# Kernel tuning notes

Hardware: AMD Instinct MI355X
Metric: run time of the kernel (lower is better)

## Reference

```python
import jax, jax.numpy as jnp
import numpy as np

N = 100000   # nodes
E = 1600000  # edges (avg degree 16)
F_IN, H, C = 128, 64, 40


def setup_inputs() -> dict:
    key = jax.random.key(0)
    ks = jax.random.split(key, 10)
    s = 0.05
    return {
        "x": jax.random.normal(ks[0], (N, F_IN), jnp.float32),
        "edge_index": jax.random.randint(ks[1], (2, E), 0, N, dtype=jnp.int32),
        "W0": jax.random.normal(ks[2], (F_IN, H), jnp.float32) * s,
        "b0": jnp.zeros((H,), jnp.float32),
        "W1": jax.random.normal(ks[3], (H, H), jnp.float32) * s,
        "b1": jnp.zeros((H,), jnp.float32),
        "W2": jax.random.normal(ks[4], (H, H), jnp.float32) * s,
        "b2": jnp.zeros((H,), jnp.float32),
        "W3": jax.random.normal(ks[5], (H, C), jnp.float32) * s,
        "b3": jnp.zeros((C,), jnp.float32),
    }


def reference(x, edge_index, W0, b0, W1, b1, W2, b2, W3, b3):
    # PyG GCNConv: add self-loops, symmetric normalization deg^-1/2 A deg^-1/2.
    loops = jnp.arange(N, dtype=edge_index.dtype)
    src = jnp.concatenate([edge_index[0], loops])  # message sources (x_j)
    dst = jnp.concatenate([edge_index[1], loops])  # aggregation targets
    deg = jax.ops.segment_sum(jnp.ones_like(dst, dtype=x.dtype), dst, num_segments=N)
    dinv = jnp.where(deg > 0, jax.lax.rsqrt(deg), 0.0)
    norm = dinv[src] * dinv[dst]  # [E+N]

    def conv(h, W, b):
        h = h @ W                                   # transform first (fewer bytes moved)
        msg = h[src] * norm[:, None]                # gather + scale
        return jax.ops.segment_sum(msg, dst, num_segments=N) + b

    h = jax.nn.leaky_relu(conv(x, W0, b0))
    h = jax.nn.leaky_relu(conv(h, W1, b1))
    h = jax.nn.leaky_relu(conv(h, W2, b2))
    h = conv(h, W3, b3)
    return jax.nn.softmax(h, axis=1)
```

## Files before the change

kernel.cpp:

```cpp
#include <hip/hip_runtime.h>
#include <hip/hip_fp16.h>
#include <math.h>


#define BBITS 9
#define BSIZE 512
#define BCAP 10240
#define CHUNK 2048
#define STAGE_CAP 12288

typedef __attribute__((ext_vector_type(8))) _Float16 half8;
typedef __attribute__((ext_vector_type(4))) float f32x4;

__global__ __launch_bounds__(256) void passA_kernel(const int* __restrict__ src, const int* __restrict__ dst,
                                                    int* gCursor, unsigned* __restrict__ pairbuf,
                                                    int nE, int nPassA,
                                                    const float* __restrict__ W0, const float* __restrict__ W1,
                                                    const float* __restrict__ W2, const float* __restrict__ W3,
                                                    __half* __restrict__ Wt0, __half* __restrict__ Wt1,
                                                    __half* __restrict__ Wt2, __half* __restrict__ Wt3) {
    const int t = threadIdx.x;
    if (blockIdx.x >= nPassA) {
        const int b = blockIdx.x - nPassA;
        if (b < 3) {
            const float* W = (b == 0) ? W0 : (b == 1) ? W1 : W2;
            __half* Wt = (b == 0) ? Wt0 : (b == 1) ? Wt1 : Wt2;
            const int K = (b == 0) ? 128 : 64;
            const int tot = 64 * K;
            for (int i = t; i < tot; i += 256) {
                int nn = i / K, k = i - nn * K;
                Wt[i] = (__half)W[k * 64 + nn];
            }
        } else {
            for (int i = t; i < 48 * 64; i += 256) {
                int c = i >> 6, k = i & 63;
                Wt3[i] = (c < 40) ? (__half)W3[k * 40 + c] : (__half)0.f;
            }
        }
        return;
    }
    __shared__ int hist[256], base[256], offs[256];
    hist[t] = 0; offs[t] = 0;
    __syncthreads();
    const int e0 = blockIdx.x * CHUNK;
    #pragma unroll
    for (int i = 0; i < CHUNK / 256; ++i) {
        int e = e0 + i * 256 + t;
        if (e < nE) atomicAdd(&hist[dst[e] >> BBITS], 1);
    }
    __syncthreads();
    if (hist[t]) base[t] = atomicAdd(&gCursor[t], hist[t]);
    __syncthreads();
    #pragma unroll
    for (int i = 0; i < CHUNK / 256; ++i) {
        int e = e0 + i * 256 + t;
        if (e < nE) {
            int d = dst[e];
            int b = d >> BBITS;
            int pos = b * BCAP + base[b] + atomicAdd(&offs[b], 1);
            pairbuf[pos] = (unsigned)src[e] | ((unsigned)(d & (BSIZE - 1)) << 17);
        }
    }
}

__global__ __launch_bounds__(256) void passB_kernel(const unsigned* __restrict__ pairbuf, const int* __restrict__ gCursor,
                                                    int* __restrict__ rowbeg, int* __restrict__ rowend,
                                                    float* __restrict__ dinv, int* __restrict__ adj, int n) {
    __shared__ unsigned stage[STAGE_CAP];
    __shared__ int cnt[BSIZE], rb[BSIZE], cur[BSIZE];
    __shared__ int sb[256];
    const int t = threadIdx.x;
    const int b = blockIdx.x;
    const int pBeg = b * BCAP;
    const int m = gCursor[b];
    cnt[t] = 0; cnt[t + 256] = 0; cur[t] = 0; cur[t + 256] = 0;
    __syncthreads();
    const bool useStage = (m <= STAGE_CAP);
    for (int i = t; i < m; i += 256) {
        unsigned p = pairbuf[pBeg + i];
        if (useStage) stage[i] = p;
        atomicAdd(&cnt[p >> 17], 1);
    }
    __syncthreads();
    const int c0 = cnt[2 * t], c1 = cnt[2 * t + 1];
    const int pairSum = c0 + c1;
    sb[t] = pairSum;
    __syncthreads();
    for (int off = 1; off < 256; off <<= 1) {
        int u = (t >= off) ? sb[t - off] : 0;
        __syncthreads();
        sb[t] += u;
        __syncthreads();
    }
    const int excl = sb[t] - pairSum;
    rb[2 * t] = excl;
    rb[2 * t + 1] = excl + c0;
    __syncthreads();
    const int nodeBase = b << BBITS;
    for (int local = t; local < BSIZE; local += 256) {
        int node = nodeBase + local;
        if (node < n) {
            int beg = pBeg + rb[local];
            rowbeg[node] = beg;
            rowend[node] = beg + cnt[local];
            dinv[node] = rsqrtf((float)(cnt[local] + 1));
        }
    }
    for (int i = t; i < m; i += 256) {
        unsigned p = useStage ? stage[i] : pairbuf[pBeg + i];
        int local = (int)(p >> 17);
        int s = (int)(p & 0x1FFFF);
        int pos = pBeg + rb[local] + atomicAdd(&cur[local], 1);
        adj[pos] = s;
    }
}

template<int K, bool AF32>
__global__ __launch_bounds__(256) void gemm_mfma_kernel(const void* __restrict__ Xv, const __half* __restrict__ Wt,
                                                        const float* __restrict__ dinv, __half* __restrict__ T, int n) {
    __shared__ __half sOut[4][16][72];
    const int tid = threadIdx.x;
    const int w = tid >> 6;
    const int l = tid & 63;
    const int l15 = l & 15;
    const int kg = l >> 4;
    const int rowBase = blockIdx.x * 64 + w * 16;

    f32x4 acc0 = {0.f, 0.f, 0.f, 0.f};
    f32x4 acc1 = acc0, acc2 = acc0, acc3 = acc0;

    const int m = rowBase + l15;
    const int mc = (m < n) ? m : (n - 1);

    for (int kc = 0; kc < K / 32; ++kc) {
        const int kb = kc * 32 + kg * 8;
        half8 a;
        if constexpr (AF32) {
            const float* Xp = (const float*)Xv + (long)mc * K + kb;
            const float4 f0 = *reinterpret_cast<const float4*>(Xp);
            const float4 f1 = *reinterpret_cast<const float4*>(Xp + 4);
            a[0] = (_Float16)f0.x; a[1] = (_Float16)f0.y; a[2] = (_Float16)f0.z; a[3] = (_Float16)f0.w;
            a[4] = (_Float16)f1.x; a[5] = (_Float16)f1.y; a[6] = (_Float16)f1.z; a[7] = (_Float16)f1.w;
        } else {
            a = *reinterpret_cast<const half8*>((const __half*)Xv + (long)mc * K + kb);
        }
        const half8 b0 = *reinterpret_cast<const half8*>(Wt + (long)(0 * 16 + l15) * K + kb);
        const half8 b1 = *reinterpret_cast<const half8*>(Wt + (long)(1 * 16 + l15) * K + kb);
        const half8 b2 = *reinterpret_cast<const half8*>(Wt + (long)(2 * 16 + l15) * K + kb);
        const half8 b3 = *reinterpret_cast<const half8*>(Wt + (long)(3 * 16 + l15) * K + kb);
        acc0 = __builtin_amdgcn_mfma_f32_16x16x32_f16(a, b0, acc0, 0, 0, 0);
        acc1 = __builtin_amdgcn_mfma_f32_16x16x32_f16(a, b1, acc1, 0, 0, 0);
        acc2 = __builtin_amdgcn_mfma_f32_16x16x32_f16(a, b2, acc2, 0, 0, 0);
        acc3 = __builtin_amdgcn_mfma_f32_16x16x32_f16(a, b3, acc3, 0, 0, 0);
    }

    float di[4];
    #pragma unroll
    for (int r = 0; r < 4; ++r) {
        const int mr = rowBase + kg * 4 + r;
        di[r] = dinv[(mr < n) ? mr : (n - 1)];
    }
    #pragma unroll
    for (int r = 0; r < 4; ++r) {
        sOut[w][kg * 4 + r][0 * 16 + l15] = (__half)(acc0[r] * di[r]);
        sOut[w][kg * 4 + r][1 * 16 + l15] = (__half)(acc1[r] * di[r]);
        sOut[w][kg * 4 + r][2 * 16 + l15] = (__half)(acc2[r] * di[r]);
        sOut[w][kg * 4 + r][3 * 16 + l15] = (__half)(acc3[r] * di[r]);
    }
    __syncthreads();
    const int srow = l >> 2;
    const int scol = (l & 3) * 16;
    const int gm = rowBase + srow;
    if (gm < n) {
        const uint4 q0 = *reinterpret_cast<const uint4*>(&sOut[w][srow][scol]);
        const uint4 q1 = *reinterpret_cast<const uint4*>(&sOut[w][srow][scol + 8]);
        *reinterpret_cast<uint4*>(&T[(long)gm * 64 + scol]) = q0;
        *reinterpret_cast<uint4*>(&T[(long)gm * 64 + scol + 8]) = q1;
    }
}

__global__ __launch_bounds__(256) void gemm3_mfma_kernel(const __half* __restrict__ X, const __half* __restrict__ Wt3,
                                                         const float* __restrict__ dinv, __half* __restrict__ T3, int n) {
    __shared__ __half sOut[4][16][72];
    const int tid = threadIdx.x;
    const int w = tid >> 6;
    const int l = tid & 63;
    const int l15 = l & 15;
    const int kg = l >> 4;
    const int rowBase = blockIdx.x * 64 + w * 16;

    f32x4 acc0 = {0.f, 0.f, 0.f, 0.f};
    f32x4 acc1 = acc0, acc2 = acc0;
    const int m = rowBase + l15;
    const int mc = (m < n) ? m : (n - 1);

    #pragma unroll
    for (int kc = 0; kc < 2; ++kc) {
        const int kb = kc * 32 + kg * 8;
        const half8 a = *reinterpret_cast<const half8*>(X + (long)mc * 64 + kb);
        const half8 b0 = *reinterpret_cast<const half8*>(Wt3 + (long)(0 * 16 + l15) * 64 + kb);
        const half8 b1 = *reinterpret_cast<const half8*>(Wt3 + (long)(1 * 16 + l15) * 64 + kb);
        const half8 b2 = *reinterpret_cast<const half8*>(Wt3 + (long)(2 * 16 + l15) * 64 + kb);
        acc0 = __builtin_amdgcn_mfma_f32_16x16x32_f16(a, b0, acc0, 0, 0, 0);
        acc1 = __builtin_amdgcn_mfma_f32_16x16x32_f16(a, b1, acc1, 0, 0, 0);
        acc2 = __builtin_amdgcn_mfma_f32_16x16x32_f16(a, b2, acc2, 0, 0, 0);
    }

    float di[4];
    #pragma unroll
    for (int r = 0; r < 4; ++r) {
        const int mr = rowBase + kg * 4 + r;
        di[r] = dinv[(mr < n) ? mr : (n - 1)];
    }
    #pragma unroll
    for (int r = 0; r < 4; ++r) {
        sOut[w][kg * 4 + r][0 * 16 + l15] = (__half)(acc0[r] * di[r]);
        sOut[w][kg * 4 + r][1 * 16 + l15] = (__half)(acc1[r] * di[r]);
        sOut[w][kg * 4 + r][2 * 16 + l15] = (__half)(acc2[r] * di[r]);
    }
    __syncthreads();
    const int srow = l >> 2;
    const int p = l & 3;
    const int gm = rowBase + srow;
    if (gm < n) {
        const uint4 q = *reinterpret_cast<const uint4*>(&sOut[w][srow][p * 8]);
        *reinterpret_cast<uint4*>(&T3[(long)gm * 40 + p * 8]) = q;
        if (p == 0) {
            const uint4 q2 = *reinterpret_cast<const uint4*>(&sOut[w][srow][32]);
            *reinterpret_cast<uint4*>(&T3[(long)gm * 40 + 32]) = q2;
        }
    }
}

__device__ __forceinline__ void accum_row(const uint4& r, __half2& x0, __half2& x1, __half2& x2, __half2& x3) {
    const __half2* v = reinterpret_cast<const __half2*>(&r);
    x0 = __hadd2(x0, v[0]); x1 = __hadd2(x1, v[1]);
    x2 = __hadd2(x2, v[2]); x3 = __hadd2(x3, v[3]);
}

template<int CHS, bool SOFTMAX>
__global__ __launch_bounds__(256) void agg_kernel(const __half* __restrict__ Tp, const float* __restrict__ dinv,
                                                  const int* __restrict__ rowbeg, const int* __restrict__ rowend,
                                                  const int* __restrict__ adj,
                                                  const float* __restrict__ bias, void* __restrict__ outp, int n) {
    const int tid = threadIdx.x;
    const int c = tid & 7;
    const int d = (int)((blockIdx.x * 256 + tid) >> 3);
    if (d >= n) return;
    const bool act = (CHS == 8) || (c < CHS);
    const int cc = act ? c : (CHS - 1);
    const uint4* Tp4 = reinterpret_cast<const uint4*>(Tp);

    __half2 a0 = __float2half2_rn(0.f), a1 = a0, a2 = a0, a3 = a0;
    __half2 c0 = a0, c1 = a0, c2 = a0, c3 = a0;
    const int beg = rowbeg[d], end = rowend[d];

    int e0 = beg;
    for (; e0 + 8 <= end; e0 += 8) {
        const int myadj = adj[e0 + c];
        uint4 r[8];
        #pragma unroll
        for (int j = 0; j < 8; ++j) {
            const int s = __shfl(myadj, j, 8);
            r[j] = Tp4[(long)s * CHS + cc];
        }
        accum_row(r[0], a0, a1, a2, a3);
        accum_row(r[1], c0, c1, c2, c3);
        accum_row(r[2], a0, a1, a2, a3);
        accum_row(r[3], c0, c1, c2, c3);
        accum_row(r[4], a0, a1, a2, a3);
        accum_row(r[5], c0, c1, c2, c3);
        accum_row(r[6], a0, a1, a2, a3);
        accum_row(r[7], c0, c1, c2, c3);
    }
    if (e0 < end) {
        const int last = end - 1;
        const int idx = e0 + c;
        const int myadj = adj[idx <= last ? idx : last];
        uint4 r[8];
        #pragma unroll
        for (int j = 0; j < 8; ++j) {
            const int s = __shfl(myadj, j, 8);
            r[j] = Tp4[(long)s * CHS + cc];
        }
        #pragma unroll
        for (int j = 0; j < 8; ++j) {
            if (e0 + j <= last) {
                if (j & 1) accum_row(r[j], c0, c1, c2, c3);
                else       accum_row(r[j], a0, a1, a2, a3);
            }
        }
    }

    float vals[8];
    if (act) {
        const uint4 sraw = Tp4[(long)d * CHS + c];
        const __half2* sh = reinterpret_cast<const __half2*>(&sraw);
        a0 = __hadd2(__hadd2(a0, c0), sh[0]);
        a1 = __hadd2(__hadd2(a1, c1), sh[1]);
        a2 = __hadd2(__hadd2(a2, c2), sh[2]);
        a3 = __hadd2(__hadd2(a3, c3), sh[3]);
        const float di = dinv[d];
        const float4 b0 = *reinterpret_cast<const float4*>(&bias[c * 8]);
        const float4 b1 = *reinterpret_cast<const float4*>(&bias[c * 8 + 4]);
        const float2 f0 = __half22float2(a0), f1 = __half22float2(a1);
        const float2 f2 = __half22float2(a2), f3 = __half22float2(a3);
        vals[0] = f0.x * di + b0.x; vals[1] = f0.y * di + b0.y;
        vals[2] = f1.x * di + b0.z; vals[3] = f1.y * di + b0.w;
        vals[4] = f2.x * di + b1.x; vals[5] = f2.y * di + b1.y;
        vals[6] = f3.x * di + b1.z; vals[7] = f3.y * di + b1.w;
    }

    if constexpr (!SOFTMAX) {
        if (act) {
            union { __half h[8]; uint4 u; } p;
            #pragma unroll
            for (int j = 0; j < 8; ++j) {
                const float v = vals[j];
                p.h[j] = (__half)(v > 0.f ? v : 0.01f * v);
            }
            *reinterpret_cast<uint4*>(&((__half*)outp)[(long)d * 64 + c * 8]) = p.u;
        }
    } else {
        float mx = -1e30f;
        if (act) {
            #pragma unroll
            for (int j = 0; j < 8; ++j) mx = fmaxf(mx, vals[j]);
        }
        #pragma unroll
        for (int off = 1; off <= 4; off <<= 1) mx = fmaxf(mx, __shfl_xor(mx, off, 8));
        float e8[8];
        float sum = 0.f;
        if (act) {
            #pragma unroll
            for (int j = 0; j < 8; ++j) { e8[j] = expf(vals[j] - mx); sum += e8[j]; }
        }
        #pragma unroll
        for (int off = 1; off <= 4; off <<= 1) sum += __shfl_xor(sum, off, 8);
        if (act) {
            const float inv = 1.0f / sum;
            float* out = (float*)outp;
            const float4 o0 = make_float4(e8[0] * inv, e8[1] * inv, e8[2] * inv, e8[3] * inv);
            const float4 o1 = make_float4(e8[4] * inv, e8[5] * inv, e8[6] * inv, e8[7] * inv);
            *reinterpret_cast<float4*>(&out[(long)d * 40 + c * 8]) = o0;
            *reinterpret_cast<float4*>(&out[(long)d * 40 + c * 8 + 4]) = o1;
        }
    }
}

extern "C" void kernel_launch(void* const* d_in, const int* in_sizes, int n_in,
                              void* d_out, int out_size, void* d_ws, size_t ws_size,
                              hipStream_t stream) {
    const float* x  = (const float*)d_in[0];
    const int*   ei = (const int*)d_in[1];
    const float* W0 = (const float*)d_in[2];
    const float* b0 = (const float*)d_in[3];
    const float* W1 = (const float*)d_in[4];
    const float* b1 = (const float*)d_in[5];
    const float* W2 = (const float*)d_in[6];
    const float* b2 = (const float*)d_in[7];
    const float* W3 = (const float*)d_in[8];
    const float* b3 = (const float*)d_in[9];

    const int N = in_sizes[0] / 128;
    const int E = in_sizes[1] / 2;
    const int* src = ei;
    const int* dst = ei + E;

    const int nBuck = (N + BSIZE - 1) >> BBITS;

    char* ws = (char*)d_ws;
    auto align256 = [](size_t v) { return (v + 255) & ~(size_t)255; };
    size_t o = 0;
    int*    gCursor    = (int*)(ws + o);    o += align256(256 * 4);
    int*    rowbeg     = (int*)(ws + o);    o += align256((size_t)N * 4);
    int*    rowend     = (int*)(ws + o);    o += align256((size_t)N * 4);
    float*  dinv       = (float*)(ws + o);  o += align256((size_t)N * 4);
    int*    adj        = (int*)(ws + o);    o += align256((size_t)nBuck * BCAP * 4);
    __half* Wt0        = (__half*)(ws + o); o += align256(64 * 128 * 2);
    __half* Wt1        = (__half*)(ws + o); o += align256(64 * 64 * 2);
    __half* Wt2        = (__half*)(ws + o); o += align256(64 * 64 * 2);
    __half* Wt3        = (__half*)(ws + o); o += align256(48 * 64 * 2);
    __half* T          = (__half*)(ws + o); o += align256((size_t)N * 64 * 2);
    __half* B          = (__half*)(ws + o); o += align256((size_t)N * 64 * 2);
    unsigned* pairbuf  = (unsigned*)T;
    float* OUT         = (float*)d_out;

    const int nb_mfma  = (N + 63) / 64;
    const int nb_agg   = (N * 8 + 255) / 256;
    const int nb_passA = (E + CHUNK - 1) / CHUNK;

    hipMemsetAsync(gCursor, 0, 1024, stream);
    passA_kernel<<<nb_passA + 4, 256, 0, stream>>>(src, dst, gCursor, pairbuf, E, nb_passA,
                                                   W0, W1, W2, W3, Wt0, Wt1, Wt2, Wt3);
    passB_kernel<<<nBuck, 256, 0, stream>>>(pairbuf, gCursor, rowbeg, rowend, dinv, adj, N);

    gemm_mfma_kernel<128, true><<<nb_mfma, 256, 0, stream>>>(x, Wt0, dinv, T, N);
    agg_kernel<8, false><<<nb_agg, 256, 0, stream>>>(T, dinv, rowbeg, rowend, adj, b0, B, N);
    gemm_mfma_kernel<64, false><<<nb_mfma, 256, 0, stream>>>(B, Wt1, dinv, T, N);
    agg_kernel<8, false><<<nb_agg, 256, 0, stream>>>(T, dinv, rowbeg, rowend, adj, b1, B, N);
    gemm_mfma_kernel<64, false><<<nb_mfma, 256, 0, stream>>>(B, Wt2, dinv, T, N);
    agg_kernel<8, false><<<nb_agg, 256, 0, stream>>>(T, dinv, rowbeg, rowend, adj, b2, B, N);
    gemm3_mfma_kernel<<<nb_mfma, 256, 0, stream>>>(B, Wt3, dinv, T, N);
    agg_kernel<5, true><<<nb_agg, 256, 0, stream>>>(T, dinv, rowbeg, rowend, adj, b3, OUT, N);
}
```

Before: 238.9 us.

## Fuse aggregation with the next layer's GEMM and stage edges in LDS

Each hidden-layer aggregation kernel now also runs the next layer's 64-wide MFMA transform from LDS and writes the dinv-scaled T directly. This removes three separate GEMM launches and the round trip of the intermediate activations through global memory. passA also caches src/dst in shared memory so they are read only once, and writes pairbuf with nontemporal stores. The cost is smaller 32-node blocks, extra LDS and syncs, and ping-pong buffer aliasing that has to stay correct.

```diff
diff --git a/kernel.cpp b/kernel.cpp
--- a/kernel.cpp
+++ b/kernel.cpp
@@ -40,25 +40,34 @@
         return;
     }
     __shared__ int hist[256], base[256], offs[256];
+    __shared__ int sdst[CHUNK], ssrc[CHUNK];
     hist[t] = 0; offs[t] = 0;
     __syncthreads();
     const int e0 = blockIdx.x * CHUNK;
     #pragma unroll
     for (int i = 0; i < CHUNK / 256; ++i) {
-        int e = e0 + i * 256 + t;
-        if (e < nE) atomicAdd(&hist[dst[e] >> BBITS], 1);
+        const int li = i * 256 + t;
+        const int e = e0 + li;
+        if (e < nE) {
+            const int d = dst[e];
+            sdst[li] = d;
+            ssrc[li] = src[e];
+            atomicAdd(&hist[d >> BBITS], 1);
+        }
     }
     __syncthreads();
     if (hist[t]) base[t] = atomicAdd(&gCursor[t], hist[t]);
     __syncthreads();
     #pragma unroll
     for (int i = 0; i < CHUNK / 256; ++i) {
-        int e = e0 + i * 256 + t;
+        const int li = i * 256 + t;
+        const int e = e0 + li;
         if (e < nE) {
-            int d = dst[e];
-            int b = d >> BBITS;
-            int pos = b * BCAP + base[b] + atomicAdd(&offs[b], 1);
-            pairbuf[pos] = (unsigned)src[e] | ((unsigned)(d & (BSIZE - 1)) << 17);
+            const int d = sdst[li];
+            const int b = d >> BBITS;
+            const int pos = b * BCAP + base[b] + atomicAdd(&offs[b], 1);
+            const unsigned pk = (unsigned)ssrc[li] | ((unsigned)(d & (BSIZE - 1)) << 17);
+            __builtin_nontemporal_store(pk, &pairbuf[pos]);
         }
     }
 }
@@ -115,9 +124,9 @@
     }
 }
 
-template<int K, bool AF32>
-__global__ __launch_bounds__(256) void gemm_mfma_kernel(const void* __restrict__ Xv, const __half* __restrict__ Wt,
-                                                        const float* __restrict__ dinv, __half* __restrict__ T, int n) {
+__global__ __launch_bounds__(256) void gemm0_kernel(const float* __restrict__ X, const __half* __restrict__ Wt,
+                                                    const float* __restrict__ dinv, __half* __restrict__ T, int n) {
+    constexpr int K = 128;
     __shared__ __half sOut[4][16][72];
     const int tid = threadIdx.x;
     const int w = tid >> 6;
@@ -128,22 +137,17 @@
 
     f32x4 acc0 = {0.f, 0.f, 0.f, 0.f};
     f32x4 acc1 = acc0, acc2 = acc0, acc3 = acc0;
-
     const int m = rowBase + l15;
     const int mc = (m < n) ? m : (n - 1);
 
     for (int kc = 0; kc < K / 32; ++kc) {
         const int kb = kc * 32 + kg * 8;
+        const float* Xp = X + (long)mc * K + kb;
+        const float4 f0 = *reinterpret_cast<const float4*>(Xp);
+        const float4 f1 = *reinterpret_cast<const float4*>(Xp + 4);
         half8 a;
-        if constexpr (AF32) {
-            const float* Xp = (const float*)Xv + (long)mc * K + kb;
-            const float4 f0 = *reinterpret_cast<const float4*>(Xp);
-            const float4 f1 = *reinterpret_cast<const float4*>(Xp + 4);
-            a[0] = (_Float16)f0.x; a[1] = (_Float16)f0.y; a[2] = (_Float16)f0.z; a[3] = (_Float16)f0.w;
-            a[4] = (_Float16)f1.x; a[5] = (_Float16)f1.y; a[6] = (_Float16)f1.z; a[7] = (_Float16)f1.w;
-        } else {
-            a = *reinterpret_cast<const half8*>((const __half*)Xv + (long)mc * K + kb);
-        }
+        a[0] = (_Float16)f0.x; a[1] = (_Float16)f0.y; a[2] = (_Float16)f0.z; a[3] = (_Float16)f0.w;
+        a[4] = (_Float16)f1.x; a[5] = (_Float16)f1.y; a[6] = (_Float16)f1.z; a[7] = (_Float16)f1.w;
         const half8 b0 = *reinterpret_cast<const half8*>(Wt + (long)(0 * 16 + l15) * K + kb);
         const half8 b1 = *reinterpret_cast<const half8*>(Wt + (long)(1 * 16 + l15) * K + kb);
         const half8 b2 = *reinterpret_cast<const half8*>(Wt + (long)(2 * 16 + l15) * K + kb);
@@ -179,82 +183,172 @@
     }
 }
 
-__global__ __launch_bounds__(256) void gemm3_mfma_kernel(const __half* __restrict__ X, const __half* __restrict__ Wt3,
-                                                         const float* __restrict__ dinv, __half* __restrict__ T3, int n) {
-    __shared__ __half sOut[4][16][72];
+__device__ __forceinline__ void accum_row(const uint4& r, __half2& x0, __half2& x1, __half2& x2, __half2& x3) {
+    const __half2* v = reinterpret_cast<const __half2*>(&r);
+    x0 = __hadd2(x0, v[0]); x1 = __hadd2(x1, v[1]);
+    x2 = __hadd2(x2, v[2]); x3 = __hadd2(x3, v[3]);
+}
+
+template<int OUTC>
+__global__ __launch_bounds__(256) void agg_gemm_kernel(const __half* __restrict__ Tp, const float* __restrict__ dinv,
+                                                       const int* __restrict__ rowbeg, const int* __restrict__ rowend,
+                                                       const int* __restrict__ adj, const float* __restrict__ bias,
+                                                       const __half* __restrict__ Wt, __half* __restrict__ Tout, int n) {
+    __shared__ __half hl[32][72];
     const int tid = threadIdx.x;
+    const int c = tid & 7;
+    const int dl = tid >> 3;
+    const int blockbase = blockIdx.x * 32;
+    int d = blockbase + dl;
+    const bool dok = (d < n);
+    if (!dok) d = n - 1;
+    const uint4* Tp4 = reinterpret_cast<const uint4*>(Tp);
+
+    __half2 a0 = __float2half2_rn(0.f), a1 = a0, a2 = a0, a3 = a0;
+    __half2 c0 = a0, c1 = a0, c2 = a0, c3 = a0;
+    const int beg = rowbeg[d], end = rowend[d];
+    int e0 = beg;
+    for (; e0 + 8 <= end; e0 += 8) {
+        const int myadj = adj[e0 + c];
+        uint4 r[8];
+        #pragma unroll
+        for (int j = 0; j < 8; ++j) {
+            const int s = __shfl(myadj, j, 8);
+            r[j] = Tp4[(long)s * 8 + c];
+        }
+        accum_row(r[0], a0, a1, a2, a3);
+        accum_row(r[1], c0, c1, c2, c3);
+        accum_row(r[2], a0, a1, a2, a3);
+        accum_row(r[3], c0, c1, c2, c3);
+        accum_row(r[4], a0, a1, a2, a3);
+        accum_row(r[5], c0, c1, c2, c3);
+        accum_row(r[6], a0, a1, a2, a3);
+        accum_row(r[7], c0, c1, c2, c3);
+    }
+    if (e0 < end) {
+        const int last = end - 1;
+        const int idx = e0 + c;
+        const int myadj = adj[idx <= last ? idx : last];
+        uint4 r[8];
+        #pragma unroll
+        for (int j = 0; j < 8; ++j) {
+            const int s = __shfl(myadj, j, 8);
+            r[j] = Tp4[(long)s * 8 + c];
+        }
+        #pragma unroll
+        for (int j = 0; j < 8; ++j) {
+            if (e0 + j <= last) {
+                if (j & 1) accum_row(r[j], c0, c1, c2, c3);
+                else       accum_row(r[j], a0, a1, a2, a3);
+            }
+        }
+    }
+    {
+        const uint4 sraw = Tp4[(long)d * 8 + c];
+        const __half2* sh = reinterpret_cast<const __half2*>(&sraw);
+        a0 = __hadd2(__hadd2(a0, c0), sh[0]);
+        a1 = __hadd2(__hadd2(a1, c1), sh[1]);
+        a2 = __hadd2(__hadd2(a2, c2), sh[2]);
+        a3 = __hadd2(__hadd2(a3, c3), sh[3]);
+        const float di = dinv[d];
+        const float4 b0 = *reinterpret_cast<const float4*>(&bias[c * 8]);
+        const float4 b1 = *reinterpret_cast<const float4*>(&bias[c * 8 + 4]);
+        const float2 f0 = __half22float2(a0), f1 = __half22float2(a1);
+        const float2 f2 = __half22float2(a2), f3 = __half22float2(a3);
+        float vals[8];
+        vals[0] = f0.x * di + b0.x; vals[1] = f0.y * di + b0.y;
+        vals[2] = f1.x * di + b0.z; vals[3] = f1.y * di + b0.w;
+        vals[4] = f2.x * di + b1.x; vals[5] = f2.y * di + b1.y;
+        vals[6] = f3.x * di + b1.z; vals[7] = f3.y * di + b1.w;
+        union { __half h[8]; uint4 u; } ph;
+        #pragma unroll
+        for (int j = 0; j < 8; ++j) {
+            const float v = vals[j];
+            ph.h[j] = (__half)(v > 0.f ? v : 0.01f * v);
+        }
+        *reinterpret_cast<uint4*>(&hl[dl][c * 8]) = ph.u;
+    }
+    __syncthreads();
+
     const int w = tid >> 6;
     const int l = tid & 63;
     const int l15 = l & 15;
     const int kg = l >> 4;
-    const int rowBase = blockIdx.x * 64 + w * 16;
-
-    f32x4 acc0 = {0.f, 0.f, 0.f, 0.f};
-    f32x4 acc1 = acc0, acc2 = acc0;
-    const int m = rowBase + l15;
-    const int mc = (m < n) ? m : (n - 1);
-
-    #pragma unroll
-    for (int kc = 0; kc < 2; ++kc) {
-        const int kb = kc * 32 + kg * 8;
-        const half8 a = *reinterpret_cast<const half8*>(X + (long)mc * 64 + kb);
-        const half8 b0 = *reinterpret_cast<const half8*>(Wt3 + (long)(0 * 16 + l15) * 64 + kb);
-        const half8 b1 = *reinterpret_cast<const half8*>(Wt3 + (long)(1 * 16 + l15) * 64 + kb);
-        const half8 b2 = *reinterpret_cast<const half8*>(Wt3 + (long)(2 * 16 + l15) * 64 + kb);
-        acc0 = __builtin_amdgcn_mfma_f32_16x16x32_f16(a, b0, acc0, 0, 0, 0);
-        acc1 = __builtin_amdgcn_mfma_f32_16x16x32_f16(a, b1, acc1, 0, 0, 0);
-        acc2 = __builtin_amdgcn_mfma_f32_16x16x32_f16(a, b2, acc2, 0, 0, 0);
+    const int ng = (w >> 1) * 16;
+    const int colbase = (w & 1) * 32;
+    const int ncg = (OUTC == 64) ? 2 : ((w & 1) ? 1 : 2);
+
+    const half8 af0 = *reinterpret_cast<const half8*>(&hl[ng + l15][0 * 32 + kg * 8]);
+    const half8 af1 = *reinterpret_cast<const half8*>(&hl[ng + l15][1 * 32 + kg * 8]);
+    half8 bf[2][2];
+    #pragma unroll
+    for (int cg = 0; cg < 2; ++cg) {
+        if (cg < ncg) {
+            #pragma unroll
+            for (int kc = 0; kc < 2; ++kc)
+                bf[cg][kc] = *reinterpret_cast<const half8*>(&Wt[(long)(colbase + cg * 16 + l15) * 64 + kc * 32 + kg * 8]);
+        }
+    }
+    __syncthreads();
+
+    f32x4 dacc[2];
+    dacc[0] = (f32x4){0.f, 0.f, 0.f, 0.f};
+    dacc[1] = (f32x4){0.f, 0.f, 0.f, 0.f};
+    #pragma unroll
+    for (int cg = 0; cg < 2; ++cg) {
+        if (cg < ncg) {
+            dacc[cg] = __builtin_amdgcn_mfma_f32_16x16x32_f16(af0, bf[cg][0], dacc[cg], 0, 0, 0);
+            dacc[cg] = __builtin_amdgcn_mfma_f32_16x16x32_f16(af1, bf[cg][1], dacc[cg], 0, 0, 0);
+        }
     }
 
     float di[4];
     #pragma unroll
     for (int r = 0; r < 4; ++r) {
-        const int mr = rowBase + kg * 4 + r;
-        di[r] = dinv[(mr < n) ? mr : (n - 1)];
-    }
-    #pragma unroll
-    for (int r = 0; r < 4; ++r) {
-        sOut[w][kg * 4 + r][0 * 16 + l15] = (__half)(acc0[r] * di[r]);
-        sOut[w][kg * 4 + r][1 * 16 + l15] = (__half)(acc1[r] * di[r]);
-        sOut[w][kg * 4 + r][2 * 16 + l15] = (__half)(acc2[r] * di[r]);
-    }
-    __syncthreads();
-    const int srow = l >> 2;
-    const int p = l & 3;
-    const int gm = rowBase + srow;
-    if (gm < n) {
-        const uint4 q = *reinterpret_cast<const uint4*>(&sOut[w][srow][p * 8]);
-        *reinterpret_cast<uint4*>(&T3[(long)gm * 40 + p * 8]) = q;
-        if (p == 0) {
-            const uint4 q2 = *reinterpret_cast<const uint4*>(&sOut[w][srow][32]);
-            *reinterpret_cast<uint4*>(&T3[(long)gm * 40 + 32]) = q2;
-        }
-    }
-}
-
-__device__ __forceinline__ void accum_row(const uint4& r, __half2& x0, __half2& x1, __half2& x2, __half2& x3) {
-    const __half2* v = reinterpret_cast<const __half2*>(&r);
-    x0 = __hadd2(x0, v[0]); x1 = __hadd2(x1, v[1]);
-    x2 = __hadd2(x2, v[2]); x3 = __hadd2(x3, v[3]);
-}
-
-template<int CHS, bool SOFTMAX>
-__global__ __launch_bounds__(256) void agg_kernel(const __half* __restrict__ Tp, const float* __restrict__ dinv,
-                                                  const int* __restrict__ rowbeg, const int* __restrict__ rowend,
-                                                  const int* __restrict__ adj,
-                                                  const float* __restrict__ bias, void* __restrict__ outp, int n) {
+        const int nd = blockbase + ng + kg * 4 + r;
+        di[r] = dinv[(nd < n) ? nd : (n - 1)];
+    }
+    #pragma unroll
+    for (int cg = 0; cg < 2; ++cg) {
+        if (cg < ncg) {
+            #pragma unroll
+            for (int r = 0; r < 4; ++r)
+                hl[ng + kg * 4 + r][colbase + cg * 16 + l15] = (__half)(dacc[cg][r] * di[r]);
+        }
+    }
+    __syncthreads();
+
+    if constexpr (OUTC == 64) {
+        const int r = tid >> 3, ch = tid & 7;
+        if (blockbase + r < n)
+            *reinterpret_cast<uint4*>(&Tout[(long)(blockbase + r) * 64 + ch * 8]) =
+                *reinterpret_cast<const uint4*>(&hl[r][ch * 8]);
+    } else {
+        if (tid < 160) {
+            const int r = tid / 5, ch = tid - 5 * r;
+            if (blockbase + r < n)
+                *reinterpret_cast<uint4*>(&Tout[(long)(blockbase + r) * 40 + ch * 8]) =
+                    *reinterpret_cast<const uint4*>(&hl[r][ch * 8]);
+        }
+    }
+}
+
+__global__ __launch_bounds__(256) void agg_sm_kernel(const __half* __restrict__ Tp, const float* __restrict__ dinv,
+                                                     const int* __restrict__ rowbeg, const int* __restrict__ rowend,
+                                                     const int* __restrict__ adj,
+                                                     const float* __restrict__ bias, float* __restrict__ out, int n) {
+    constexpr int CHS = 5;
     const int tid = threadIdx.x;
     const int c = tid & 7;
     const int d = (int)((blockIdx.x * 256 + tid) >> 3);
     if (d >= n) return;
-    const bool act = (CHS == 8) || (c < CHS);
+    const bool act = (c < CHS);
     const int cc = act ? c : (CHS - 1);
     const uint4* Tp4 = reinterpret_cast<const uint4*>(Tp);
 
     __half2 a0 = __float2half2_rn(0.f), a1 = a0, a2 = a0, a3 = a0;
     __half2 c0 = a0, c1 = a0, c2 = a0, c3 = a0;
     const int beg = rowbeg[d], end = rowend[d];
-
     int e0 = beg;
     for (; e0 + 8 <= end; e0 += 8) {
         const int myadj = adj[e0 + c];
@@ -310,41 +404,27 @@
         vals[4] = f2.x * di + b1.x; vals[5] = f2.y * di + b1.y;
         vals[6] = f3.x * di + b1.z; vals[7] = f3.y * di + b1.w;
     }
-
-    if constexpr (!SOFTMAX) {
-        if (act) {
-            union { __half h[8]; uint4 u; } p;
-            #pragma unroll
-            for (int j = 0; j < 8; ++j) {
-                const float v = vals[j];
-                p.h[j] = (__half)(v > 0.f ? v : 0.01f * v);
-            }
-            *reinterpret_cast<uint4*>(&((__half*)outp)[(long)d * 64 + c * 8]) = p.u;
-        }
-    } else {
-        float mx = -1e30f;
-        if (act) {
-            #pragma unroll
-            for (int j = 0; j < 8; ++j) mx = fmaxf(mx, vals[j]);
-        }
-        #pragma unroll
-        for (int off = 1; off <= 4; off <<= 1) mx = fmaxf(mx, __shfl_xor(mx, off, 8));
-        float e8[8];
-        float sum = 0.f;
-        if (act) {
-            #pragma unroll
-            for (int j = 0; j < 8; ++j) { e8[j] = expf(vals[j] - mx); sum += e8[j]; }
-        }
-        #pragma unroll
-        for (int off = 1; off <= 4; off <<= 1) sum += __shfl_xor(sum, off, 8);
-        if (act) {
-            const float inv = 1.0f / sum;
-            float* out = (float*)outp;
-            const float4 o0 = make_float4(e8[0] * inv, e8[1] * inv, e8[2] * inv, e8[3] * inv);
-            const float4 o1 = make_float4(e8[4] * inv, e8[5] * inv, e8[6] * inv, e8[7] * inv);
-            *reinterpret_cast<float4*>(&out[(long)d * 40 + c * 8]) = o0;
-            *reinterpret_cast<float4*>(&out[(long)d * 40 + c * 8 + 4]) = o1;
-        }
+    float mx = -1e30f;
+    if (act) {
+        #pragma unroll
+        for (int j = 0; j < 8; ++j) mx = fmaxf(mx, vals[j]);
+    }
+    #pragma unroll
+    for (int off = 1; off <= 4; off <<= 1) mx = fmaxf(mx, __shfl_xor(mx, off, 8));
+    float e8[8];
+    float sum = 0.f;
+    if (act) {
+        #pragma unroll
+        for (int j = 0; j < 8; ++j) { e8[j] = expf(vals[j] - mx); sum += e8[j]; }
+    }
+    #pragma unroll
+    for (int off = 1; off <= 4; off <<= 1) sum += __shfl_xor(sum, off, 8);
+    if (act) {
+        const float inv = 1.0f / sum;
+        const float4 o0 = make_float4(e8[0] * inv, e8[1] * inv, e8[2] * inv, e8[3] * inv);
+        const float4 o1 = make_float4(e8[4] * inv, e8[5] * inv, e8[6] * inv, e8[7] * inv);
+        *reinterpret_cast<float4*>(&out[(long)d * 40 + c * 8]) = o0;
+        *reinterpret_cast<float4*>(&out[(long)d * 40 + c * 8 + 4]) = o1;
     }
 }
 
@@ -386,8 +466,9 @@
     unsigned* pairbuf  = (unsigned*)T;
     float* OUT         = (float*)d_out;
 
-    const int nb_mfma  = (N + 63) / 64;
-    const int nb_agg   = (N * 8 + 255) / 256;
+    const int nb_gemm0 = (N + 63) / 64;
+    const int nb_fused = (N + 31) / 32;
+    const int nb_aggsm = (N * 8 + 255) / 256;
     const int nb_passA = (E + CHUNK - 1) / CHUNK;
 
     hipMemsetAsync(gCursor, 0, 1024, stream);
@@ -395,12 +476,9 @@
                                                    W0, W1, W2, W3, Wt0, Wt1, Wt2, Wt3);
     passB_kernel<<<nBuck, 256, 0, stream>>>(pairbuf, gCursor, rowbeg, rowend, dinv, adj, N);
 
-    gemm_mfma_kernel<128, true><<<nb_mfma, 256, 0, stream>>>(x, Wt0, dinv, T, N);
-    agg_kernel<8, false><<<nb_agg, 256, 0, stream>>>(T, dinv, rowbeg, rowend, adj, b0, B, N);
-    gemm_mfma_kernel<64, false><<<nb_mfma, 256, 0, stream>>>(B, Wt1, dinv, T, N);
-    agg_kernel<8, false><<<nb_agg, 256, 0, stream>>>(T, dinv, rowbeg, rowend, adj, b1, B, N);
-    gemm_mfma_kernel<64, false><<<nb_mfma, 256, 0, stream>>>(B, Wt2, dinv, T, N);
-    agg_kernel<8, false><<<nb_agg, 256, 0, stream>>>(T, dinv, rowbeg, rowend, adj, b2, B, N);
-    gemm3_mfma_kernel<<<nb_mfma, 256, 0, stream>>>(B, Wt3, dinv, T, N);
-    agg_kernel<5, true><<<nb_agg, 256, 0, stream>>>(T, dinv, rowbeg, rowend, adj, b3, OUT, N);
-}
+    gemm0_kernel<<<nb_gemm0, 256, 0, stream>>>(x, Wt0, dinv, T, N);
+    agg_gemm_kernel<64><<<nb_fused, 256, 0, stream>>>(T, dinv, rowbeg, rowend, adj, b0, Wt1, B, N);
+    agg_gemm_kernel<64><<<nb_fused, 256, 0, stream>>>(B, dinv, rowbeg, rowend, adj, b1, Wt2, T, N);
+    agg_gemm_kernel<48><<<nb_fused, 256, 0, stream>>>(T, dinv, rowbeg, rowend, adj, b2, Wt3, B, N);
+    agg_sm_kernel<<<nb_aggsm, 256, 0, stream>>>(B, dinv, rowbeg, rowend, adj, b3, OUT, N);
+}
```

New measurement: 242.5 us. No clear change (+1.5%).
